# Kernel optimization log

Measured on AMD Instinct MI355X. Metric: run time of the kernel, lower is better.

The kernel has to match this reference:

```python
import jax, jax.numpy as jnp
import numpy as np

RPN_BATCHSIZE = 256
RPN_FG_FRACTION = 0.5
STRIDE = 16
NEG_OVERLAP = 0.3
POS_OVERLAP = 0.7
ALLOWED_BORDER = 0.0


def _base_anchors(base_size=16, ratios=(0.5, 1.0, 2.0), scales=(8, 16, 32)):
    cx = cy = (base_size - 1) / 2.0
    size = float(base_size * base_size)
    out = []
    for r in ratios:
        ws = round(np.sqrt(size / r))
        hs = round(ws * r)
        for s in scales:
            W, H = ws * s, hs * s
            out.append([cx - (W - 1) / 2.0, cy - (H - 1) / 2.0,
                        cx + (W - 1) / 2.0, cy + (H - 1) / 2.0])
    return jnp.asarray(np.array(out, dtype=np.float32))


def _all_anchors(rr, cc, stride):
    # keras_rcnn.backend.shift((rr, cc), stride) -> (rr*cc*9, 4)
    base = _base_anchors()
    sx = jnp.arange(rr, dtype=jnp.float32) * stride
    sy = jnp.arange(cc, dtype=jnp.float32) * stride
    SX, SY = jnp.meshgrid(sx, sy)  # 'xy' indexing as in keras-rcnn
    shifts = jnp.stack([SX.ravel(), SY.ravel(), SX.ravel(), SY.ravel()], axis=1)
    return (shifts[:, None, :] + base[None, :, :]).reshape(-1, 4)


def _overlap(a, b):
    # pairwise IoU with the +1 pixel convention; a: (N,4), b: (G,4) -> (N,G)
    area_a = (a[:, 2] - a[:, 0] + 1.0) * (a[:, 3] - a[:, 1] + 1.0)
    area_b = (b[:, 2] - b[:, 0] + 1.0) * (b[:, 3] - b[:, 1] + 1.0)
    iw = jnp.maximum(jnp.minimum(a[:, None, 2], b[None, :, 2]) - jnp.maximum(a[:, None, 0], b[None, :, 0]) + 1.0, 0.0)
    ih = jnp.maximum(jnp.minimum(a[:, None, 3], b[None, :, 3]) - jnp.maximum(a[:, None, 1], b[None, :, 1]) + 1.0, 0.0)
    inter = iw * ih
    return inter / (area_a[:, None] + area_b[None, :] - inter)


def _bbox_transform(ex, gt):
    # keras_rcnn.backend.bbox_transform: (dx, dy, dw, dh) with +1 convention
    ew = ex[:, 2] - ex[:, 0] + 1.0
    eh = ex[:, 3] - ex[:, 1] + 1.0
    ecx = ex[:, 0] + 0.5 * ew
    ecy = ex[:, 1] + 0.5 * eh
    gw = gt[:, 2] - gt[:, 0] + 1.0
    gh = gt[:, 3] - gt[:, 1] + 1.0
    gcx = gt[:, 0] + 0.5 * gw
    gcy = gt[:, 1] + 0.5 * gh
    return jnp.stack([(gcx - ecx) / ew, (gcy - ecy) / eh,
                      jnp.log(gw / ew), jnp.log(gh / eh)], axis=1)


def _subsample(labels, value, max_keep, key):
    # randomly demote labels==value to -1 (don't care) so at most max_keep remain;
    # jit-friendly equivalent of shuffle + scatter in the original.
    mask = labels == value
    r = jnp.where(mask, jax.random.uniform(key, labels.shape), -1.0)
    rank = jnp.argsort(jnp.argsort(-r))  # rank 0 = highest random score
    keep = jnp.minimum(jnp.sum(mask), max_keep)
    return jnp.where(mask & (rank >= keep), -1.0, labels)


def _anchor_target(scores, gt_boxes, metadata):
    meta = metadata[0]          # (height, width, scale)
    gt = gt_boxes[0]            # (G, 4)
    rr, cc = scores.shape[1], scores.shape[2]
    anchors = _all_anchors(rr, cc, STRIDE)  # (N, 4)
    inside = ((anchors[:, 0] >= -ALLOWED_BORDER) & (anchors[:, 1] >= -ALLOWED_BORDER)
              & (anchors[:, 2] < ALLOWED_BORDER + meta[1])
              & (anchors[:, 3] < ALLOWED_BORDER + meta[0]))
    overlaps = _overlap(anchors, gt)                     # (N, G)
    overlaps = jnp.where(inside[:, None], overlaps, -1.0)
    argmax_inds = jnp.argmax(overlaps, axis=1)           # best gt per anchor
    max_ov = jnp.take_along_axis(overlaps, argmax_inds[:, None], axis=1)[:, 0]
    gt_argmax = jnp.argmax(overlaps, axis=0)             # best anchor per gt
    labels = jnp.full((anchors.shape[0],), -1.0, dtype=jnp.float32)
    # clobber_positives=False: negatives first
    labels = jnp.where(inside & (max_ov < NEG_OVERLAP), 0.0, labels)
    # unique + scatter_add in the original just sets these entries to 1
    labels = labels.at[gt_argmax].set(1.0)
    labels = jnp.where(max_ov >= POS_OVERLAP, 1.0, labels)
    # balance: at most 128 positives, then fill to 256 with negatives
    k1, k2 = jax.random.split(jax.random.key(42))
    labels = _subsample(labels, 1.0, int(RPN_FG_FRACTION * RPN_BATCHSIZE), k1)
    n_pos = jnp.sum(labels == 1.0)
    labels = _subsample(labels, 0.0, RPN_BATCHSIZE - n_pos, k2)
    targets = _bbox_transform(anchors, gt[argmax_inds])
    targets = jnp.where(inside[:, None], targets, 0.0)   # unmap with fill=0
    return labels[None, :], targets[None, :, :]


def setup_inputs() -> dict:
    key = jax.random.key(0)
    k1, k2, k3 = jax.random.split(key, 3)
    scores = jax.random.normal(k1, (1, 128, 128, 18), dtype=jnp.float32)
    # valid GT boxes inside a 2048x2048 image: x1<x2, y1<y2
    xy = jax.random.uniform(k2, (1, 128, 2), minval=0.0, maxval=1800.0)
    wh = jax.random.uniform(k3, (1, 128, 2), minval=16.0, maxval=240.0)
    gt_boxes = jnp.concatenate([xy, xy + wh], axis=-1)
    metadata = jnp.ones((1, 3), dtype=jnp.float32) * jnp.array([2048.0, 2048.0, 1.0], dtype=jnp.float32)
    return {"scores": scores, "gt_boxes": gt_boxes, "metadata": metadata}


def reference(scores, gt_boxes, metadata):
    return _anchor_target(scores, gt_boxes, metadata)
```

## Files before the change

kernel.cpp:

```cpp
#include <hip/hip_runtime.h>
#include <stdint.h>

#define N_ANCH 147456
#define NGT 128

#define W_CNTS   0
#define W_SEL    1152
#define W_GMAX2  1160
#define W_LCNT   3208
#define W_LIST   4360
#define MAXSURV  2048

__constant__ float c_base[9][4] = {
  {-84.f,-40.f,99.f,55.f},
  {-176.f,-88.f,191.f,103.f},
  {-360.f,-184.f,375.f,199.f},
  {-56.f,-56.f,71.f,71.f},
  {-120.f,-120.f,135.f,135.f},
  {-248.f,-248.f,263.f,263.f},
  {-36.f,-80.f,51.f,95.f},
  {-80.f,-168.f,95.f,183.f},
  {-168.f,-344.f,183.f,359.f},
};
__constant__ float c_areaA[9] = {
  17664.f, 70656.f, 282624.f,
  16384.f, 65536.f, 262144.f,
  15488.f, 61952.f, 247808.f,
};

__host__ __device__ inline uint32_t rotl32(uint32_t v, int d){ return (v<<d)|(v>>(32-d)); }

__host__ __device__ inline void tf2x32(uint32_t k0, uint32_t k1, uint32_t x0, uint32_t x1,
                                       uint32_t* o0, uint32_t* o1){
  uint32_t ks0=k0, ks1=k1, ks2=k0^k1^0x1BD11BDAu;
  x0 += ks0; x1 += ks1;
  #define TFR(r) { x0 += x1; x1 = rotl32(x1,(r)); x1 ^= x0; }
  TFR(13) TFR(15) TFR(26) TFR(6)   x0+=ks1; x1+=ks2+1u;
  TFR(17) TFR(29) TFR(16) TFR(24)  x0+=ks2; x1+=ks0+2u;
  TFR(13) TFR(15) TFR(26) TFR(6)   x0+=ks0; x1+=ks1+3u;
  TFR(17) TFR(29) TFR(16) TFR(24)  x0+=ks1; x1+=ks2+4u;
  TFR(13) TFR(15) TFR(26) TFR(6)   x0+=ks2; x1+=ks0+5u;
  #undef TFR
  *o0=x0; *o1=x1;
}

__device__ inline uint32_t rand_m23(uint32_t k0, uint32_t k1, uint32_t j){
  uint32_t a, b;
  tf2x32(k0, k1, 0u, j, &a, &b);
  return (a ^ b) >> 9;
}

__global__ __launch_bounds__(256) void kA(const float* __restrict__ gt,
                                          const float* __restrict__ meta,
                                          signed char* __restrict__ lab,
                                          uint32_t* __restrict__ keys,
                                          uint32_t* __restrict__ ctl,
                                          float* __restrict__ out,
                                          uint32_t pk0,uint32_t pk1,
                                          uint32_t nk0,uint32_t nk1){
  int bid = blockIdx.x;
  float W = meta[1], H = meta[0];
  if (bid < 576){
    __shared__ float4 sg[NGT];
    __shared__ float  sB[NGT];
    __shared__ uint32_t slist[NGT];
    __shared__ unsigned long long sball[2];
    __shared__ uint32_t c0, c1;
    if (threadIdx.x == 0){ c0 = 0u; c1 = 0u; }
    for (int t = threadIdx.x; t < NGT; t += 256){
      float4 G = reinterpret_cast<const float4*>(gt)[t];
      sg[t] = G;
      sB[t] = __fmul_rn(G.z - G.x + 1.0f, G.w - G.y + 1.0f);
    }
    int i0 = bid*256, k0 = i0/9, k1 = (i0+255)/9;
    int y0 = k0 >> 7, y1 = k1 >> 7;
    int x0 = (y0==y1) ? (k0 & 127) : 0, x1 = (y0==y1) ? (k1 & 127) : 127;
    float Rxlo = 16.f*x0 - 361.f, Rxhi = 16.f*x1 + 376.f;
    float Rylo = 16.f*y0 - 345.f, Ryhi = 16.f*y1 + 360.f;
    __syncthreads();
    if (threadIdx.x < NGT){
      float4 G = sg[threadIdx.x];
      bool rel = (G.x <= Rxhi) && (G.z >= Rxlo) && (G.y <= Ryhi) && (G.w >= Rylo);
      unsigned long long b = __ballot(rel);
      if ((threadIdx.x & 63) == 0) sball[threadIdx.x >> 6] = b;
    }
    __syncthreads();
    unsigned long long b0 = sball[0], b1 = sball[1];
    if (threadIdx.x < NGT){
      float4 G = sg[threadIdx.x];
      bool rel = (G.x <= Rxhi) && (G.z >= Rxlo) && (G.y <= Ryhi) && (G.w >= Rylo);
      if (rel){
        int lane = threadIdx.x & 63;
        unsigned long long my = (threadIdx.x < 64) ? b0 : b1;
        uint32_t pos = (uint32_t)__popcll(my & ((1ull << lane) - 1ull));
        if (threadIdx.x >= 64) pos += (uint32_t)__popcll(b0);
        slist[pos] = (uint32_t)threadIdx.x;
      }
    }
    __syncthreads();
    int nl = (int)(__popcll(b0) + __popcll(b1));
    int fs;
    {
      unsigned long long n0 = ~b0;
      if (n0) fs = __ffsll((long long)n0) - 1;
      else { unsigned long long n1 = ~b1; fs = n1 ? 64 + __ffsll((long long)n1) - 1 : 128; }
    }
    int i = bid*256 + threadIdx.x;
    int k = i / 9; int t9 = i - k*9;
    float sx = 16.0f * (float)(k & 127);
    float sy = 16.0f * (float)(k >> 7);
    float ax1 = c_base[t9][0] + sx, ay1 = c_base[t9][1] + sy;
    float ax2 = c_base[t9][2] + sx, ay2 = c_base[t9][3] + sy;
    float areaA = c_areaA[t9];
    bool inside = (ax1 >= 0.0f) && (ay1 >= 0.0f) && (ax2 < W) && (ay2 < H);
    float best = -1.0f; int arg = 0;
    if (inside){
      best = -2.0f;
      for (int li = 0; li < nl; ++li){
        int g = (int)slist[li];
        float4 G = sg[g];
        float iw = fminf(ax2,G.z) - fmaxf(ax1,G.x) + 1.0f;
        float ih = fminf(ay2,G.w) - fmaxf(ay1,G.y) + 1.0f;
        float ov = 0.0f;
        if (iw > 0.0f && ih > 0.0f){
          float inter = __fmul_rn(iw, ih);
          ov = inter / ((areaA + sB[g]) - inter);
        }
        if (ov > best){ best = ov; arg = g; }
      }
      if (best < 0.0f){ best = 0.0f; arg = fs; }
      else if (best == 0.0f){ arg = (arg < fs) ? arg : fs; }
    }
    signed char L = -1;
    if (best >= 0.7f) L = 1;
    else if (inside && best < 0.3f) L = 0;
    lab[i] = L;
    if (L == 1) keys[i] = rand_m23(pk0,pk1,(uint32_t)i);
    else if (L == 0) keys[i] = rand_m23(nk0,nk1,(uint32_t)i);
    unsigned long long q1 = __ballot(L == 1);
    unsigned long long q0 = __ballot(L == 0);
    if ((threadIdx.x & 63) == 0){
      if (q1) atomicAdd(&c0, (uint32_t)__popcll(q1));
      if (q0) atomicAdd(&c1, (uint32_t)__popcll(q0));
    }
    float4 t4 = make_float4(0.f, 0.f, 0.f, 0.f);
    if (inside){
      float4 G = sg[arg];
      float ew = ax2-ax1+1.0f, eh = ay2-ay1+1.0f;
      float ecx = ax1 + 0.5f*ew, ecy = ay1 + 0.5f*eh;
      float gw = G.z-G.x+1.0f, gh = G.w-G.y+1.0f;
      float gcx = G.x + 0.5f*gw, gcy = G.y + 0.5f*gh;
      t4.x = (gcx-ecx)/ew; t4.y = (gcy-ecy)/eh;
      t4.z = logf(gw/ew);  t4.w = logf(gh/eh);
    }
    *reinterpret_cast<float4*>(out + N_ANCH + 4*(size_t)i) = t4;
    __syncthreads();
    if (threadIdx.x == 0){
      ctl[W_CNTS + 2*bid]     = c0;
      ctl[W_CNTS + 2*bid + 1] = c1;
    }
  } else {
    int b2 = bid - 576;
    int g = b2 >> 3, slice = b2 & 7;
    float bx1=gt[4*g], by1=gt[4*g+1], bx2=gt[4*g+2], by2=gt[4*g+3];
    float areaB = __fmul_rn(bx2-bx1+1.0f, by2-by1+1.0f);
    int pxl = max(0,   (int)ceilf ((bx1 - 377.0f) * 0.0625f));
    int pxh = min(127, (int)floorf((bx2 + 362.0f) * 0.0625f));
    int pyl = max(0,   (int)ceilf ((by1 - 361.0f) * 0.0625f));
    int pyh = min(127, (int)floorf((by2 + 346.0f) * 0.0625f));
    uint32_t Wp = (uint32_t)(pxh - pxl + 1);
    int tot = (int)Wp * (pyh - pyl + 1);
    uint32_t mdiv = (4194304u + Wp - 1u) / Wp;
    float a0[9],a1[9],a2[9],a3[9];
    #pragma unroll
    for (int t=0;t<9;++t){ a0[t]=c_base[t][0]; a1[t]=c_base[t][1];
                           a2[t]=c_base[t][2]; a3[t]=c_base[t][3]; }
    float best = -2.0f; int bi = 0;
    for (int pos = slice*256 + threadIdx.x; pos < tot; pos += 2048){
      uint32_t dq = (uint32_t)(((unsigned long long)(uint32_t)pos * mdiv) >> 22);
      int py = pyl + (int)dq;
      int px = pxl + (int)((uint32_t)pos - dq * Wp);
      int k = (py << 7) + px;
      float sx = 16.0f * (float)px;
      float sy = 16.0f * (float)py;
      #pragma unroll
      for (int t = 0; t < 9; ++t){
        float ax1=a0[t]+sx, ay1=a1[t]+sy, ax2=a2[t]+sx, ay2=a3[t]+sy;
        bool inside = (ax1 >= 0.0f) && (ay1 >= 0.0f) && (ax2 < W) && (ay2 < H);
        float iw = fminf(ax2,bx2) - fmaxf(ax1,bx1) + 1.0f;
        float ih = fminf(ay2,by2) - fmaxf(ay1,by1) + 1.0f;
        float ov = inside ? 0.0f : -1.0f;
        if (inside && iw > 0.0f && ih > 0.0f){
          float inter = __fmul_rn(iw, ih);
          ov = inter / ((c_areaA[t] + areaB) - inter);
        }
        if (ov > best){ best = ov; bi = k*9 + t; }
      }
    }
    unsigned long long p = 0ull;
    if (best >= 0.0f)
      p = ((unsigned long long)__float_as_uint(best) << 32) | (uint32_t)(~(uint32_t)bi);
    __shared__ unsigned long long sred[256];
    sred[threadIdx.x] = p;
    __syncthreads();
    for (int s = 128; s > 0; s >>= 1){
      if ((int)threadIdx.x < s){
        unsigned long long q = sred[threadIdx.x + s];
        if (q > sred[threadIdx.x]) sred[threadIdx.x] = q;
      }
      __syncthreads();
    }
    if (threadIdx.x == 0)
      reinterpret_cast<unsigned long long*>(ctl + W_GMAX2)[b2] = sred[0];
  }
}

__global__ __launch_bounds__(256) void kC(const signed char* __restrict__ lab,
                                          const uint32_t* __restrict__ keys,
                                          float* __restrict__ out,
                                          uint32_t* __restrict__ ctl,
                                          uint32_t pk0, uint32_t pk1){
  int tid = threadIdx.x, bid = blockIdx.x;
  __shared__ uint32_t widx[NGT], wkey[NGT], wflag[256];
  __shared__ int sdP, sdN;
  __shared__ unsigned long long red[256];
  __shared__ uint32_t sel[6];
  __shared__ uint32_t lcnt[2];
  wflag[tid] = 0xFFFFFFFFu;
  if (tid == 0){ sdP = 0; sdN = 0; lcnt[0] = 0u; lcnt[1] = 0u; }
  if (tid < NGT){
    const unsigned long long* g2 =
      reinterpret_cast<const unsigned long long*>(ctl + W_GMAX2);
    unsigned long long best = 0ull;
    #pragma unroll
    for (int s = 0; s < 8; ++s){
      unsigned long long q = g2[tid*8 + s];
      if (q > best) best = q;
    }
    uint32_t idx = best ? ~(uint32_t)best : 0xFFFFFFFFu;
    widx[tid] = idx;
    wkey[tid] = (idx != 0xFFFFFFFFu) ? rand_m23(pk0, pk1, idx) : 0u;
  }
  unsigned long long acc = 0ull;
  for (int b = tid; b < 576; b += 256)
    acc += ((unsigned long long)ctl[W_CNTS + 2*b] << 32) | ctl[W_CNTS + 2*b + 1];
  red[tid] = acc;
  __syncthreads();
  for (int s = 128; s > 0; s >>= 1){
    if (tid < s) red[tid] += red[tid + s];
    __syncthreads();
  }
  if (tid < NGT && widx[tid] != 0xFFFFFFFFu){
    uint32_t idx = widx[tid];
    if ((idx >> 8) == (uint32_t)bid) wflag[idx & 255u] = wkey[tid];
    bool resp = true;
    for (int g = 0; g < tid; ++g) if (widx[g] == idx){ resp = false; break; }
    if (resp){
      int oldL = lab[idx];
      if (oldL != 1){ atomicAdd(&sdP, 1); if (oldL == 0) atomicAdd(&sdN, 1); }
    }
  }
  __syncthreads();
  if (tid == 0){
    uint32_t cntP = (uint32_t)(red[0] >> 32) + (uint32_t)sdP;
    uint32_t cntN = (uint32_t)red[0] - (uint32_t)sdN;
    uint32_t keepP = cntP < 128u ? cntP : 128u;
    uint32_t keepN = cntN < (256u - keepP) ? cntN : (256u - keepP);
    uint32_t cnts[2] = {cntP, cntN}, keeps[2] = {keepP, keepN};
    for (int c = 0; c < 2; ++c){
      uint32_t cnt = cnts[c], keep = keeps[c];
      uint32_t all = (keep >= cnt) ? 1u : 0u, Tf = 0u;
      if (!all){
        unsigned long long slack = 2ull * keep;
        if (slack < cnt)
          Tf = (uint32_t)((((unsigned long long)(cnt - slack)) << 23) / cnt);
      }
      sel[c*3+0] = Tf; sel[c*3+1] = keep; sel[c*3+2] = all;
    }
    if (bid == 0){
      for (int c = 0; c < 2; ++c){
        ctl[W_SEL + c*4 + 0] = sel[c*3+0];
        ctl[W_SEL + c*4 + 1] = sel[c*3+1];
        ctl[W_SEL + c*4 + 2] = sel[c*3+2];
      }
    }
  }
  __syncthreads();
  int i = bid*256 + tid;
  int L = lab[i];
  uint32_t wf = wflag[tid];
  uint32_t m = 0u;
  if (wf != 0xFFFFFFFFu){ L = 1; m = wf; }
  else if (L >= 0) m = keys[i];
  if (L < 0){
    out[i] = -1.0f;
  } else {
    int ch = (L == 1) ? 0 : 1;
    if (sel[ch*3+2]){
      out[i] = (float)L;
    } else if (m < sel[ch*3+0]){
      out[i] = -1.0f;
    } else {
      uint32_t pos = atomicAdd(&lcnt[ch], 1u);
      reinterpret_cast<unsigned long long*>(ctl + W_LIST)
        [(ch*576 + bid)*256 + pos] =
        ((unsigned long long)(m ^ 0x7FFFFFu) << 32) | (uint32_t)i;
    }
  }
  __syncthreads();
  if (tid < 2) ctl[W_LCNT + tid*576 + bid] = lcnt[tid];
}

__global__ __launch_bounds__(1024) void kD(float* __restrict__ out,
                                           uint32_t* __restrict__ ctl){
  int tid = threadIdx.x;
  __shared__ unsigned long long skey[MAXSURV];
  __shared__ uint32_t scan[1024];
  for (int c = 0; c < 2; ++c){
    uint32_t keep    = ctl[W_SEL + c*4 + 1];
    uint32_t keepAll = ctl[W_SEL + c*4 + 2];
    if (!keepAll){
      uint32_t cnum = (tid < 576) ? ctl[W_LCNT + c*576 + tid] : 0u;
      scan[tid] = cnum;
      __syncthreads();
      for (int off = 1; off < 1024; off <<= 1){
        uint32_t v = (tid >= off) ? scan[tid - off] : 0u;
        __syncthreads();
        scan[tid] += v;
        __syncthreads();
      }
      int n = (int)scan[1023]; if (n > MAXSURV) n = MAXSURV;
      if (cnum){
        uint32_t base = scan[tid] - cnum;
        const unsigned long long* list =
          reinterpret_cast<const unsigned long long*>(ctl + W_LIST)
          + (size_t)(c*576 + tid)*256;
        for (uint32_t j = 0; j < cnum; ++j){
          uint32_t p = base + j;
          if (p < (uint32_t)MAXSURV) skey[p] = list[j];
        }
      }
      __syncthreads();
      float kv = (c == 0) ? 1.0f : 0.0f;
      for (int p = tid; p < n; p += 1024){
        unsigned long long mine = skey[p];
        uint32_t r = 0;
        for (int j = 0; j < n; ++j) r += (skey[j] < mine) ? 1u : 0u;
        uint32_t idx = (uint32_t)(mine & 0xFFFFFFFFull);
        out[idx] = (r < keep) ? kv : -1.0f;
      }
    }
    __syncthreads();
  }
}

extern "C" void kernel_launch(void* const* d_in, const int* in_sizes, int n_in,
                              void* d_out, int out_size, void* d_ws, size_t ws_size,
                              hipStream_t stream) {
  const float* gt   = (const float*)d_in[1];
  const float* meta = (const float*)d_in[2];
  float* out = (float*)d_out;
  signed char* lab = (signed char*)d_ws;
  uint32_t* keys = (uint32_t*)((char*)d_ws + N_ANCH);
  uint32_t* ctl  = keys + N_ANCH;

  uint32_t a0,a1,b0,b1;
  tf2x32(0u, 42u, 0u, 0u, &a0, &a1);
  tf2x32(0u, 42u, 0u, 1u, &b0, &b1);

  kA<<<1600, 256, 0, stream>>>(gt, meta, lab, keys, ctl, out, a0, a1, b0, b1);
  kC<<<576, 256, 0, stream>>>(lab, keys, out, ctl, a0, a1);
  kD<<<1, 1024, 0, stream>>>(out, ctl);
}
```

Before: 47.82 us.

## Fuse label finalize and survivor ranking into one kernel with dedicated ranking block

Merges kC and kD into a single launch of 145 blocks of 1024 threads. The first 144 blocks write final labels for anchors that need no ranking. The extra block scans all labels itself, collects survivor keys straight into shared memory, patches in the GT-argmax forced positives, and ranks them. This removes one kernel launch and the global survivor list, count arrays and scan. In exchange, one block serially scans the whole label array, and survivors per class are capped at 1024 instead of 2048.

```diff
diff --git a/kernel.cpp b/kernel.cpp
--- a/kernel.cpp
+++ b/kernel.cpp
@@ -5,11 +5,9 @@
 #define NGT 128
 
 #define W_CNTS   0
-#define W_SEL    1152
 #define W_GMAX2  1160
-#define W_LCNT   3208
-#define W_LIST   4360
-#define MAXSURV  2048
+
+typedef unsigned long long u64;
 
 __constant__ float c_base[9][4] = {
   {-84.f,-40.f,99.f,55.f},
@@ -215,52 +213,58 @@
   }
 }
 
-__global__ __launch_bounds__(256) void kC(const signed char* __restrict__ lab,
-                                          const uint32_t* __restrict__ keys,
-                                          float* __restrict__ out,
-                                          uint32_t* __restrict__ ctl,
-                                          uint32_t pk0, uint32_t pk1){
+__global__ __launch_bounds__(1024) void kC2(const signed char* __restrict__ lab,
+                                            const uint32_t* __restrict__ keys,
+                                            float* __restrict__ out,
+                                            uint32_t* __restrict__ ctl,
+                                            uint32_t pk0, uint32_t pk1){
   int tid = threadIdx.x, bid = blockIdx.x;
-  __shared__ uint32_t widx[NGT], wkey[NGT], wflag[256];
+  __shared__ uint32_t widx[NGT], wkey[NGT];
+  __shared__ signed char wraw[NGT];
+  __shared__ unsigned char respf[NGT];
+  __shared__ uint32_t wflag[1024];
+  __shared__ u64 red[1024];
   __shared__ int sdP, sdN;
-  __shared__ unsigned long long red[256];
   __shared__ uint32_t sel[6];
-  __shared__ uint32_t lcnt[2];
+  __shared__ u64 skey[2048];
+  __shared__ uint32_t nctr[2];
   wflag[tid] = 0xFFFFFFFFu;
-  if (tid == 0){ sdP = 0; sdN = 0; lcnt[0] = 0u; lcnt[1] = 0u; }
+  if (tid == 0){ sdP = 0; sdN = 0; nctr[0] = 0u; nctr[1] = 0u; }
+  u64 acc = 0ull;
+  if (tid < 576)
+    acc = ((u64)ctl[W_CNTS + 2*tid] << 32) | ctl[W_CNTS + 2*tid + 1];
+  red[tid] = acc;
   if (tid < NGT){
-    const unsigned long long* g2 =
-      reinterpret_cast<const unsigned long long*>(ctl + W_GMAX2);
-    unsigned long long best = 0ull;
+    const u64* g2 = reinterpret_cast<const u64*>(ctl + W_GMAX2);
+    u64 best = 0ull;
     #pragma unroll
     for (int s = 0; s < 8; ++s){
-      unsigned long long q = g2[tid*8 + s];
+      u64 q = g2[tid*8 + s];
       if (q > best) best = q;
     }
     uint32_t idx = best ? ~(uint32_t)best : 0xFFFFFFFFu;
     widx[tid] = idx;
     wkey[tid] = (idx != 0xFFFFFFFFu) ? rand_m23(pk0, pk1, idx) : 0u;
   }
-  unsigned long long acc = 0ull;
-  for (int b = tid; b < 576; b += 256)
-    acc += ((unsigned long long)ctl[W_CNTS + 2*b] << 32) | ctl[W_CNTS + 2*b + 1];
-  red[tid] = acc;
   __syncthreads();
-  for (int s = 128; s > 0; s >>= 1){
-    if (tid < s) red[tid] += red[tid + s];
-    __syncthreads();
-  }
-  if (tid < NGT && widx[tid] != 0xFFFFFFFFu){
+  if (tid < NGT){
     uint32_t idx = widx[tid];
-    if ((idx >> 8) == (uint32_t)bid) wflag[idx & 255u] = wkey[tid];
-    bool resp = true;
-    for (int g = 0; g < tid; ++g) if (widx[g] == idx){ resp = false; break; }
-    if (resp){
-      int oldL = lab[idx];
-      if (oldL != 1){ atomicAdd(&sdP, 1); if (oldL == 0) atomicAdd(&sdN, 1); }
-    }
+    unsigned char rp = 0; signed char rl = -1;
+    if (idx != 0xFFFFFFFFu){
+      if (bid < 144 && (idx >> 10) == (uint32_t)bid) wflag[idx & 1023u] = wkey[tid];
+      bool resp = true;
+      for (int g = 0; g < tid; ++g) if (widx[g] == idx){ resp = false; break; }
+      rl = lab[idx];
+      rp = resp ? 1 : 0;
+      if (resp && rl != 1){ atomicAdd(&sdP, 1); if (rl == 0) atomicAdd(&sdN, 1); }
+    }
+    respf[tid] = rp; wraw[tid] = rl;
   }
   __syncthreads();
+  for (int off = 512; off > 0; off >>= 1){
+    if (tid < off) red[tid] += red[tid + off];
+    __syncthreads();
+  }
   if (tid == 0){
     uint32_t cntP = (uint32_t)(red[0] >> 32) + (uint32_t)sdP;
     uint32_t cntN = (uint32_t)red[0] - (uint32_t)sdN;
@@ -271,86 +275,85 @@
       uint32_t cnt = cnts[c], keep = keeps[c];
       uint32_t all = (keep >= cnt) ? 1u : 0u, Tf = 0u;
       if (!all){
-        unsigned long long slack = 2ull * keep;
+        u64 slack = 2ull * keep;
         if (slack < cnt)
-          Tf = (uint32_t)((((unsigned long long)(cnt - slack)) << 23) / cnt);
+          Tf = (uint32_t)((((u64)(cnt - slack)) << 23) / cnt);
       }
       sel[c*3+0] = Tf; sel[c*3+1] = keep; sel[c*3+2] = all;
     }
-    if (bid == 0){
-      for (int c = 0; c < 2; ++c){
-        ctl[W_SEL + c*4 + 0] = sel[c*3+0];
-        ctl[W_SEL + c*4 + 1] = sel[c*3+1];
-        ctl[W_SEL + c*4 + 2] = sel[c*3+2];
-      }
-    }
   }
   __syncthreads();
-  int i = bid*256 + tid;
-  int L = lab[i];
-  uint32_t wf = wflag[tid];
-  uint32_t m = 0u;
-  if (wf != 0xFFFFFFFFu){ L = 1; m = wf; }
-  else if (L >= 0) m = keys[i];
-  if (L < 0){
-    out[i] = -1.0f;
-  } else {
-    int ch = (L == 1) ? 0 : 1;
-    if (sel[ch*3+2]){
-      out[i] = (float)L;
-    } else if (m < sel[ch*3+0]){
+  if (bid < 144){
+    int i = bid*1024 + tid;
+    int L = lab[i];
+    uint32_t wf = wflag[tid];
+    uint32_t m = 0u;
+    if (wf != 0xFFFFFFFFu){ L = 1; m = wf; }
+    else if (L >= 0) m = keys[i];
+    if (L < 0){
       out[i] = -1.0f;
     } else {
-      uint32_t pos = atomicAdd(&lcnt[ch], 1u);
-      reinterpret_cast<unsigned long long*>(ctl + W_LIST)
-        [(ch*576 + bid)*256 + pos] =
-        ((unsigned long long)(m ^ 0x7FFFFFu) << 32) | (uint32_t)i;
-    }
-  }
-  __syncthreads();
-  if (tid < 2) ctl[W_LCNT + tid*576 + bid] = lcnt[tid];
-}
-
-__global__ __launch_bounds__(1024) void kD(float* __restrict__ out,
-                                           uint32_t* __restrict__ ctl){
-  int tid = threadIdx.x;
-  __shared__ unsigned long long skey[MAXSURV];
-  __shared__ uint32_t scan[1024];
-  for (int c = 0; c < 2; ++c){
-    uint32_t keep    = ctl[W_SEL + c*4 + 1];
-    uint32_t keepAll = ctl[W_SEL + c*4 + 2];
-    if (!keepAll){
-      uint32_t cnum = (tid < 576) ? ctl[W_LCNT + c*576 + tid] : 0u;
-      scan[tid] = cnum;
-      __syncthreads();
-      for (int off = 1; off < 1024; off <<= 1){
-        uint32_t v = (tid >= off) ? scan[tid - off] : 0u;
-        __syncthreads();
-        scan[tid] += v;
-        __syncthreads();
-      }
-      int n = (int)scan[1023]; if (n > MAXSURV) n = MAXSURV;
-      if (cnum){
-        uint32_t base = scan[tid] - cnum;
-        const unsigned long long* list =
-          reinterpret_cast<const unsigned long long*>(ctl + W_LIST)
-          + (size_t)(c*576 + tid)*256;
-        for (uint32_t j = 0; j < cnum; ++j){
-          uint32_t p = base + j;
-          if (p < (uint32_t)MAXSURV) skey[p] = list[j];
-        }
-      }
-      __syncthreads();
+      int ch = (L == 1) ? 0 : 1;
+      if (sel[ch*3+2])           out[i] = (float)L;
+      else if (m < sel[ch*3+0])  out[i] = -1.0f;
+    }
+  } else {
+    uint32_t Tf0 = sel[0], all0 = sel[2], Tf1 = sel[3], all1 = sel[5];
+    const int4* lab4 = reinterpret_cast<const int4*>(lab);
+    for (int j = 0; j < 9; ++j){
+      int4 v = lab4[j*1024 + tid];
+      int base = (j*1024 + tid) * 16;
+      #pragma unroll
+      for (int w = 0; w < 4; ++w){
+        int wv = (w==0) ? v.x : (w==1) ? v.y : (w==2) ? v.z : v.w;
+        #pragma unroll
+        for (int b = 0; b < 4; ++b){
+          signed char L = (signed char)((wv >> (8*b)) & 0xFF);
+          if (L < 0) continue;
+          int ch = (L == 1) ? 0 : 1;
+          if (ch == 0 ? all0 : all1) continue;
+          int idx = base + w*4 + b;
+          uint32_t m = keys[idx];
+          if (m < (ch == 0 ? Tf0 : Tf1)) continue;
+          uint32_t pos = atomicAdd(&nctr[ch], 1u);
+          if (pos < 1024u)
+            skey[ch*1024 + pos] = ((u64)(m ^ 0x7FFFFFu) << 32) | (uint32_t)idx;
+        }
+      }
+    }
+    __syncthreads();
+    if (tid < NGT && respf[tid]){
+      uint32_t idx = widx[tid]; signed char rl = wraw[tid]; uint32_t wk = wkey[tid];
+      if (rl != 1){
+        if (rl == 0 && !all1 && keys[idx] >= Tf1){
+          uint32_t n1 = nctr[1]; if (n1 > 1024u) n1 = 1024u;
+          for (uint32_t p = 0; p < n1; ++p){
+            if ((uint32_t)(skey[1024 + p] & 0xFFFFFFFFull) == idx){
+              skey[1024 + p] = ~0ull; break;
+            }
+          }
+        }
+        if (!all0 && wk >= Tf0){
+          uint32_t pos = atomicAdd(&nctr[0], 1u);
+          if (pos < 1024u)
+            skey[pos] = ((u64)(wk ^ 0x7FFFFFu) << 32) | idx;
+        }
+      }
+    }
+    __syncthreads();
+    for (int c = 0; c < 2; ++c){
+      if (c == 0 ? all0 : all1) continue;
+      uint32_t keep = sel[c*3+1];
+      int n = (int)nctr[c]; if (n > 1024) n = 1024;
       float kv = (c == 0) ? 1.0f : 0.0f;
       for (int p = tid; p < n; p += 1024){
-        unsigned long long mine = skey[p];
+        u64 mine = skey[c*1024 + p];
+        if (mine == ~0ull) continue;
         uint32_t r = 0;
-        for (int j = 0; j < n; ++j) r += (skey[j] < mine) ? 1u : 0u;
-        uint32_t idx = (uint32_t)(mine & 0xFFFFFFFFull);
-        out[idx] = (r < keep) ? kv : -1.0f;
-      }
-    }
-    __syncthreads();
+        for (int q = 0; q < n; ++q) r += (skey[c*1024 + q] < mine) ? 1u : 0u;
+        out[(uint32_t)(mine & 0xFFFFFFFFull)] = (r < keep) ? kv : -1.0f;
+      }
+    }
   }
 }
 
@@ -368,7 +371,6 @@
   tf2x32(0u, 42u, 0u, 0u, &a0, &a1);
   tf2x32(0u, 42u, 0u, 1u, &b0, &b1);
 
-  kA<<<1600, 256, 0, stream>>>(gt, meta, lab, keys, ctl, out, a0, a1, b0, b1);
-  kC<<<576, 256, 0, stream>>>(lab, keys, out, ctl, a0, a1);
-  kD<<<1, 1024, 0, stream>>>(out, ctl);
-}
+  kA <<<1600, 256, 0, stream>>>(gt, meta, lab, keys, ctl, out, a0, a1, b0, b1);
+  kC2<<<145, 1024, 0, stream>>>(lab, keys, out, ctl, a0, a1);
+}
```

Result: slower. 87.73 us (+83.4%).
